# Performance work log

Measured on AMD Instinct MI355X. Metric: run time of the kernel, lower is better.

## Reference

```python
import jax, jax.numpy as jnp
import numpy as np

N_NODES = 100000
N_EDGES = 3200000
IN_FEAT = 256   # dim * decoder_heads = 128 * 2
HEADS = 2
N_CLASSES = 8
CURV = 1.0
NEG_SLOPE = 0.2
EPS = 1e-15


def setup_inputs() -> dict:
    key = jax.random.key(0)
    ks = jax.random.split(key, 7)
    x = jax.random.normal(ks[0], (N_NODES, IN_FEAT), dtype=jnp.float32) * 0.1
    edge_index = jax.random.randint(ks[1], (2, N_EDGES), 0, N_NODES, dtype=jnp.int64)
    W = jax.random.normal(ks[2], (IN_FEAT, HEADS * N_CLASSES), dtype=jnp.float32) * (1.0 / np.sqrt(IN_FEAT))
    attn_l = jax.random.normal(ks[3], (HEADS, N_CLASSES), dtype=jnp.float32) * 0.1
    attn_r = jax.random.normal(ks[4], (HEADS, N_CLASSES), dtype=jnp.float32) * 0.1
    bias = jnp.zeros((HEADS, N_CLASSES), dtype=jnp.float32)
    W_res = jax.random.normal(ks[5], (IN_FEAT, HEADS * N_CLASSES), dtype=jnp.float32) * (1.0 / np.sqrt(IN_FEAT))
    return {"x": x, "edge_index": edge_index, "W": W, "attn_l": attn_l,
            "attn_r": attn_r, "bias": bias, "W_res": W_res}


def _artanh(z):
    z = jnp.clip(z, -1.0 + 1e-7, 1.0 - 1e-7)
    return 0.5 * (jnp.log1p(z) - jnp.log1p(-z))


def _logmap0_poincare(x, c):
    # PoincareBall.logmap0; proj_tan0 is identity for the Poincare ball.
    sqrt_c = jnp.sqrt(c)
    norm = jnp.maximum(jnp.linalg.norm(x, axis=-1, keepdims=True), EPS)
    scale = _artanh(sqrt_c * norm) / (sqrt_c * norm)
    return scale * x


def reference(x, edge_index, W, attn_l, attn_r, bias, W_res):
    N = x.shape[0]
    # hyperbolic -> tangent space at origin
    h = _logmap0_poincare(x, CURV)                               # [N, F]
    # GATConv (DGL-style), dropout disabled (eval)
    feat = (h @ W).reshape(N, HEADS, N_CLASSES)                  # [N, H, C]
    el = jnp.einsum('nhc,hc->nh', feat, attn_l)                  # [N, H]
    er = jnp.einsum('nhc,hc->nh', feat, attn_r)                  # [N, H]
    src, dst = edge_index[0], edge_index[1]
    e = el[src] + er[dst]                                        # [E, H]
    e = jnp.where(e >= 0, e, NEG_SLOPE * e)                      # leaky_relu
    # edge softmax over incoming edges of each destination node
    m = jax.ops.segment_max(e, dst, num_segments=N)              # [N, H]
    m = jnp.where(jnp.isfinite(m), m, 0.0)
    e_exp = jnp.exp(e - m[dst])                                  # [E, H]
    denom = jax.ops.segment_sum(e_exp, dst, num_segments=N)      # [N, H]
    alpha = e_exp / jnp.maximum(denom[dst], EPS)                 # [E, H]
    # aggregate messages
    msg = alpha[:, :, None] * feat[src]                          # [E, H, C]
    rst = jax.ops.segment_sum(msg, dst, num_segments=N)          # [N, H, C]
    # residual + bias
    rst = rst + (h @ W_res).reshape(N, HEADS, N_CLASSES) + bias
    # Decoder.decode: probs.mean(dim=1) over heads
    return rst.mean(axis=1)                                      # [N, C]
```

## Files before the change

kernel.cpp:

```cpp
#include <hip/hip_runtime.h>
#include <math.h>

#define N_NODES 100000
#define N_EDGES 3200000
#define IN_FEAT 256
#define HEADS 2
#define NC 8
#define FH 16
#define NEG_SLOPE 0.2f
#define EPSF 1e-15f

#define BSH 7
#define BUCK_W 128
#define DLM 127
#define NBUCK ((N_NODES + BUCK_W - 1) / BUCK_W)
#define B1 256
#define EPB (N_EDGES / B1)

#define SORT_CAP 5120
#define RCAP (SORT_CAP / 256)

typedef float f32x4 __attribute__((ext_vector_type(4)));
typedef short bf16x8 __attribute__((ext_vector_type(8)));

__device__ __forceinline__ unsigned short f2bf(float f) {
    unsigned u = __float_as_uint(f);
    u += 0x7FFFu + ((u >> 16) & 1u);
    return (unsigned short)(u >> 16);
}
__device__ __forceinline__ float bflo(unsigned u) { return __uint_as_float(u << 16); }
__device__ __forceinline__ float bfhi(unsigned u) { return __uint_as_float(u & 0xFFFF0000u); }

__device__ __forceinline__ int chunk_of_block(int bid) {
    return (bid & 7) * (B1 / 8) + (bid >> 3);
}

__global__ __launch_bounds__(256) void k_node(
        const float* __restrict__ x, const float* __restrict__ W,
        const float* __restrict__ Wres, const float* __restrict__ attn_l,
        const float* __restrict__ attn_r,
        unsigned short* __restrict__ featb, float* __restrict__ res,
        float* __restrict__ el, float* __restrict__ er) {
    int wid = (blockIdx.x * 256 + threadIdx.x) >> 6;
    int n0 = wid * 16;
    if (n0 >= N_NODES) return;
    int l   = threadIdx.x & 63;
    int col = l & 15;
    int g   = l >> 4;

    bf16x8 bw[8], bq[8];
    #pragma unroll
    for (int kk = 0; kk < 8; kk++) {
        #pragma unroll
        for (int j = 0; j < 8; j++) {
            int k = kk * 32 + g * 8 + j;
            bw[kk][j] = (short)f2bf(W[k * FH + col]);
            bq[kk][j] = (short)f2bf(Wres[k * FH + col]);
        }
    }

    const float* xr = x + (size_t)(n0 + col) * IN_FEAT;
    f32x4 acc0 = {0.f, 0.f, 0.f, 0.f};
    f32x4 acc1 = {0.f, 0.f, 0.f, 0.f};
    float ss = 0.f;
    #pragma unroll
    for (int kk = 0; kk < 8; kk++) {
        float4 v0 = *(const float4*)(xr + kk * 32 + g * 8);
        float4 v1 = *(const float4*)(xr + kk * 32 + g * 8 + 4);
        ss += v0.x * v0.x + v0.y * v0.y + v0.z * v0.z + v0.w * v0.w
            + v1.x * v1.x + v1.y * v1.y + v1.z * v1.z + v1.w * v1.w;
        bf16x8 a;
        a[0] = (short)f2bf(v0.x); a[1] = (short)f2bf(v0.y);
        a[2] = (short)f2bf(v0.z); a[3] = (short)f2bf(v0.w);
        a[4] = (short)f2bf(v1.x); a[5] = (short)f2bf(v1.y);
        a[6] = (short)f2bf(v1.z); a[7] = (short)f2bf(v1.w);
        acc0 = __builtin_amdgcn_mfma_f32_16x16x32_bf16(a, bw[kk], acc0, 0, 0, 0);
        acc1 = __builtin_amdgcn_mfma_f32_16x16x32_bf16(a, bq[kk], acc1, 0, 0, 0);
    }

    ss += __shfl_xor(ss, 16);
    ss += __shfl_xor(ss, 32);
    float norm = fmaxf(sqrtf(ss), EPSF);
    float z = fminf(norm, 1.f - 1e-7f);
    float at = 0.5f * (log1pf(z) - log1pf(-z));
    float scale = at / norm;

    float alc = attn_l[col], arc = attn_r[col];

    #pragma unroll
    for (int i = 0; i < 4; i++) {
        int ri = g * 4 + i;
        float s_i = __shfl(scale, ri);
        int nr = n0 + ri;
        float f_i = acc0[i] * s_i;
        float q_i = acc1[i] * s_i;
        featb[(size_t)nr * FH + col] = f2bf(f_i);
        res  [(size_t)nr * FH + col] = q_i;
        float pl = f_i * alc, pr = f_i * arc;
        float pl0 = (col < 8) ? pl : 0.f, pl1 = (col < 8) ? 0.f : pl;
        float pr0 = (col < 8) ? pr : 0.f, pr1 = (col < 8) ? 0.f : pr;
        #pragma unroll
        for (int m = 1; m < 16; m <<= 1) {
            pl0 += __shfl_xor(pl0, m); pl1 += __shfl_xor(pl1, m);
            pr0 += __shfl_xor(pr0, m); pr1 += __shfl_xor(pr1, m);
        }
        if (col == 0) {
            *(float2*)(el + nr * 2) = make_float2(pl0, pl1);
            *(float2*)(er + nr * 2) = make_float2(pr0, pr1);
        }
    }
}

__global__ __launch_bounds__(256) void k_count(const int* __restrict__ ei,
                                               int* __restrict__ hist_g) {
    __shared__ int h[NBUCK];
    for (int i = threadIdx.x; i < NBUCK; i += 256) h[i] = 0;
    __syncthreads();
    int chunk = chunk_of_block(blockIdx.x);
    const int4* dp = (const int4*)(ei + N_EDGES + (size_t)chunk * EPB);
    for (int i = threadIdx.x; i < EPB / 4; i += 256) {
        int4 d = dp[i];
        atomicAdd(&h[d.x >> BSH], 1);
        atomicAdd(&h[d.y >> BSH], 1);
        atomicAdd(&h[d.z >> BSH], 1);
        atomicAdd(&h[d.w >> BSH], 1);
    }
    __syncthreads();
    int* outp = hist_g + (size_t)chunk * NBUCK;
    for (int i = threadIdx.x; i < NBUCK; i += 256) outp[i] = h[i];
}

__global__ __launch_bounds__(64) void k_scan1(int* __restrict__ hist_g,
                                              int* __restrict__ btot) {
    __shared__ int sm[64];
    int bucket = blockIdx.x;
    int t = threadIdx.x;
    int carry = 0;
    for (int base = 0; base < B1; base += 64) {
        int blk = base + t;
        int v = hist_g[(size_t)blk * NBUCK + bucket];
        __syncthreads();
        sm[t] = v;
        __syncthreads();
        for (int off = 1; off < 64; off <<= 1) {
            int u = (t >= off) ? sm[t - off] : 0;
            __syncthreads();
            sm[t] += u;
            __syncthreads();
        }
        hist_g[(size_t)blk * NBUCK + bucket] = carry + sm[t] - v;
        carry += sm[63];
    }
    if (t == 0) btot[bucket] = carry;
}

__global__ __launch_bounds__(1024) void k_scan2(const int* __restrict__ btot,
                                                int* __restrict__ bstart) {
    __shared__ int sm[1024];
    int t = threadIdx.x;
    int v = (t < NBUCK) ? btot[t] : 0;
    sm[t] = v;
    __syncthreads();
    for (int off = 1; off < 1024; off <<= 1) {
        int u = (t >= off) ? sm[t - off] : 0;
        __syncthreads();
        sm[t] += u;
        __syncthreads();
    }
    if (t < NBUCK) bstart[t] = sm[t] - v;
    if (t == 1023) bstart[NBUCK] = sm[1023];
}

__global__ __launch_bounds__(256) void k_scatter2(const int* __restrict__ ei,
                                                  const int* __restrict__ hist_g,
                                                  const int* __restrict__ bstart,
                                                  unsigned* __restrict__ packed) {
    __shared__ int cur[NBUCK];
    int chunk = chunk_of_block(blockIdx.x);
    const int* hrow = hist_g + (size_t)chunk * NBUCK;
    for (int i = threadIdx.x; i < NBUCK; i += 256) cur[i] = bstart[i] + hrow[i];
    __syncthreads();
    size_t e0 = (size_t)chunk * EPB;
    const int4* sp = (const int4*)(ei + e0);
    const int4* dp = (const int4*)(ei + N_EDGES + e0);
    for (int i = threadIdx.x; i < EPB / 4; i += 256) {
        int4 s = sp[i];
        int4 d = dp[i];
        int p0 = atomicAdd(&cur[d.x >> BSH], 1);
        int p1 = atomicAdd(&cur[d.y >> BSH], 1);
        int p2 = atomicAdd(&cur[d.z >> BSH], 1);
        int p3 = atomicAdd(&cur[d.w >> BSH], 1);
        packed[p0] = (unsigned)s.x | ((unsigned)(d.x & DLM) << 17);
        packed[p1] = (unsigned)s.y | ((unsigned)(d.y & DLM) << 17);
        packed[p2] = (unsigned)s.z | ((unsigned)(d.z & DLM) << 17);
        packed[p3] = (unsigned)s.w | ((unsigned)(d.w & DLM) << 17);
    }
}

__global__ __launch_bounds__(256) void k_aggsort(
        const unsigned* __restrict__ packed, const int* __restrict__ bstart,
        const float* __restrict__ el, const float* __restrict__ er,
        const unsigned short* __restrict__ featb, const float* __restrict__ res,
        const float* __restrict__ bias, float* __restrict__ out) {
    __shared__ int cnt[BUCK_W];
    __shared__ int off[BUCK_W];
    __shared__ unsigned srt[SORT_CAP];
    int b = blockIdx.x, t = threadIdx.x;
    int lo = bstart[b], hi = bstart[b + 1];

    if (t < BUCK_W) cnt[t] = 0;
    __syncthreads();

    unsigned pe[RCAP];
    int      tk[RCAP];
    #pragma unroll
    for (int i = 0; i < RCAP; i++) {
        int j = lo + i * 256 + t;
        if (j < hi) {
            unsigned p = packed[j];
            pe[i] = p;
            tk[i] = atomicAdd(&cnt[p >> 17], 1);
        } else {
            pe[i] = 0u; tk[i] = -1;
        }
    }
    __syncthreads();

    if (t < BUCK_W) off[t] = cnt[t];
    __syncthreads();
    #pragma unroll
    for (int d = 1; d < BUCK_W; d <<= 1) {
        int v = (t < BUCK_W && t >= d) ? off[t - d] : 0;
        __syncthreads();
        if (t < BUCK_W) off[t] += v;
        __syncthreads();
    }

    #pragma unroll
    for (int i = 0; i < RCAP; i++) {
        if (tk[i] >= 0) {
            int dl = (int)(pe[i] >> 17);
            srt[off[dl] - cnt[dl] + tk[i]] = pe[i] & 0x1FFFFu;
        }
    }
    __syncthreads();

    int dl = t >> 1, r = t & 1;
    int n = b * BUCK_W + dl;
    if (n >= N_NODES) return;
    int sBeg = off[dl] - cnt[dl];
    int sEnd = off[dl];
    float2 ern = *(const float2*)(er + n * 2);
    float den0 = 0.f, den1 = 0.f;
    float S[FH];
    #pragma unroll
    for (int k = 0; k < FH; k++) S[k] = 0.f;

    int j = sBeg + r;
    for (; j + 2 < sEnd; j += 4) {
        int sa = (int)srt[j], sb2 = (int)srt[j + 2];
        float2 ea = *(const float2*)(el + sa * 2);
        float2 eb = *(const float2*)(el + sb2 * 2);
        const uint4* fpa = (const uint4*)(featb + (size_t)sa * FH);
        const uint4* fpb = (const uint4*)(featb + (size_t)sb2 * FH);
        uint4 ua0 = fpa[0], ua1 = fpa[1];
        uint4 ub0 = fpb[0], ub1 = fpb[1];
        float va0 = ea.x + ern.x, va1 = ea.y + ern.y;
        float vb0 = eb.x + ern.x, vb1 = eb.y + ern.y;
        va0 = va0 >= 0.f ? va0 : NEG_SLOPE * va0;
        va1 = va1 >= 0.f ? va1 : NEG_SLOPE * va1;
        vb0 = vb0 >= 0.f ? vb0 : NEG_SLOPE * vb0;
        vb1 = vb1 >= 0.f ? vb1 : NEG_SLOPE * vb1;
        float wa0 = __expf(va0), wa1 = __expf(va1);
        float wb0 = __expf(vb0), wb1 = __expf(vb1);
        den0 += wa0 + wb0; den1 += wa1 + wb1;
        S[0]  = fmaf(wa0, bflo(ua0.x), fmaf(wb0, bflo(ub0.x), S[0]));
        S[1]  = fmaf(wa0, bfhi(ua0.x), fmaf(wb0, bfhi(ub0.x), S[1]));
        S[2]  = fmaf(wa0, bflo(ua0.y), fmaf(wb0, bflo(ub0.y), S[2]));
        S[3]  = fmaf(wa0, bfhi(ua0.y), fmaf(wb0, bfhi(ub0.y), S[3]));
        S[4]  = fmaf(wa0, bflo(ua0.z), fmaf(wb0, bflo(ub0.z), S[4]));
        S[5]  = fmaf(wa0, bfhi(ua0.z), fmaf(wb0, bfhi(ub0.z), S[5]));
        S[6]  = fmaf(wa0, bflo(ua0.w), fmaf(wb0, bflo(ub0.w), S[6]));
        S[7]  = fmaf(wa0, bfhi(ua0.w), fmaf(wb0, bfhi(ub0.w), S[7]));
        S[8]  = fmaf(wa1, bflo(ua1.x), fmaf(wb1, bflo(ub1.x), S[8]));
        S[9]  = fmaf(wa1, bfhi(ua1.x), fmaf(wb1, bfhi(ub1.x), S[9]));
        S[10] = fmaf(wa1, bflo(ua1.y), fmaf(wb1, bflo(ub1.y), S[10]));
        S[11] = fmaf(wa1, bfhi(ua1.y), fmaf(wb1, bfhi(ub1.y), S[11]));
        S[12] = fmaf(wa1, bflo(ua1.z), fmaf(wb1, bflo(ub1.z), S[12]));
        S[13] = fmaf(wa1, bfhi(ua1.z), fmaf(wb1, bfhi(ub1.z), S[13]));
        S[14] = fmaf(wa1, bflo(ua1.w), fmaf(wb1, bflo(ub1.w), S[14]));
        S[15] = fmaf(wa1, bfhi(ua1.w), fmaf(wb1, bfhi(ub1.w), S[15]));
    }
    for (; j < sEnd; j += 2) {
        int sa = (int)srt[j];
        float2 ea = *(const float2*)(el + sa * 2);
        float v0 = ea.x + ern.x, v1 = ea.y + ern.y;
        v0 = v0 >= 0.f ? v0 : NEG_SLOPE * v0;
        v1 = v1 >= 0.f ? v1 : NEG_SLOPE * v1;
        float w0 = __expf(v0), w1 = __expf(v1);
        den0 += w0; den1 += w1;
        const uint4* fp = (const uint4*)(featb + (size_t)sa * FH);
        uint4 u0 = fp[0], u1 = fp[1];
        S[0]  = fmaf(w0, bflo(u0.x), S[0]);  S[1]  = fmaf(w0, bfhi(u0.x), S[1]);
        S[2]  = fmaf(w0, bflo(u0.y), S[2]);  S[3]  = fmaf(w0, bfhi(u0.y), S[3]);
        S[4]  = fmaf(w0, bflo(u0.z), S[4]);  S[5]  = fmaf(w0, bfhi(u0.z), S[5]);
        S[6]  = fmaf(w0, bflo(u0.w), S[6]);  S[7]  = fmaf(w0, bfhi(u0.w), S[7]);
        S[8]  = fmaf(w1, bflo(u1.x), S[8]);  S[9]  = fmaf(w1, bfhi(u1.x), S[9]);
        S[10] = fmaf(w1, bflo(u1.y), S[10]); S[11] = fmaf(w1, bfhi(u1.y), S[11]);
        S[12] = fmaf(w1, bflo(u1.z), S[12]); S[13] = fmaf(w1, bfhi(u1.z), S[13]);
        S[14] = fmaf(w1, bflo(u1.w), S[14]); S[15] = fmaf(w1, bfhi(u1.w), S[15]);
    }

    #pragma unroll
    for (int k = 0; k < FH; k++) S[k] += __shfl_xor(S[k], 1);
    den0 += __shfl_xor(den0, 1);
    den1 += __shfl_xor(den1, 1);

    if (r == 0) {
        float inv0 = 1.f / fmaxf(den0, EPSF);
        float inv1 = 1.f / fmaxf(den1, EPSF);
        const float* rr = res + (size_t)n * FH;
        float4 r0a = *(const float4*)(rr + 0),  r0b = *(const float4*)(rr + 4);
        float4 r1a = *(const float4*)(rr + 8),  r1b = *(const float4*)(rr + 12);
        float4 oa, ob;
        oa.x = 0.5f * ((S[0] * inv0 + r0a.x + bias[0])  + (S[8]  * inv1 + r1a.x + bias[8]));
        oa.y = 0.5f * ((S[1] * inv0 + r0a.y + bias[1])  + (S[9]  * inv1 + r1a.y + bias[9]));
        oa.z = 0.5f * ((S[2] * inv0 + r0a.z + bias[2])  + (S[10] * inv1 + r1a.z + bias[10]));
        oa.w = 0.5f * ((S[3] * inv0 + r0a.w + bias[3])  + (S[11] * inv1 + r1a.w + bias[11]));
        ob.x = 0.5f * ((S[4] * inv0 + r0b.x + bias[4])  + (S[12] * inv1 + r1b.x + bias[12]));
        ob.y = 0.5f * ((S[5] * inv0 + r0b.y + bias[5])  + (S[13] * inv1 + r1b.y + bias[13]));
        ob.z = 0.5f * ((S[6] * inv0 + r0b.z + bias[6])  + (S[14] * inv1 + r1b.z + bias[14]));
        ob.w = 0.5f * ((S[7] * inv0 + r0b.w + bias[7])  + (S[15] * inv1 + r1b.w + bias[15]));
        *(float4*)(out + (size_t)n * NC + 0) = oa;
        *(float4*)(out + (size_t)n * NC + 4) = ob;
    }
}

extern "C" void kernel_launch(void* const* d_in, const int* in_sizes, int n_in,
                              void* d_out, int out_size, void* d_ws, size_t ws_size,
                              hipStream_t stream) {
    const float* x      = (const float*)d_in[0];
    const int*   ei     = (const int*)d_in[1];
    const float* W      = (const float*)d_in[2];
    const float* attn_l = (const float*)d_in[3];
    const float* attn_r = (const float*)d_in[4];
    const float* bias   = (const float*)d_in[5];
    const float* Wres   = (const float*)d_in[6];
    float* out = (float*)d_out;

    char* ws = (char*)d_ws;
    const size_t szFB   = (size_t)N_NODES * FH * sizeof(unsigned short);
    const size_t szNF   = (size_t)N_NODES * FH * sizeof(float);
    const size_t szNH   = (size_t)N_NODES * HEADS * sizeof(float);
    const size_t szHist = (((size_t)B1 * NBUCK * sizeof(int)) + 255) & ~(size_t)255;
    const size_t szBt   = 4096;
    size_t off = 0;
    unsigned short* featb = (unsigned short*)(ws + off); off += szFB;
    float*    res    = (float*)(ws + off); off += szNF;
    float*    el     = (float*)(ws + off); off += szNH;
    float*    er     = (float*)(ws + off); off += szNH;
    int*      hist_g = (int*)  (ws + off); off += szHist;
    int*      btot   = (int*)  (ws + off); off += szBt;
    int*      bstart = (int*)  (ws + off); off += szBt;
    unsigned* packed = (unsigned*)(ws + off); off += (size_t)N_EDGES * sizeof(unsigned);

    k_node<<<(N_NODES / 16 + 3) / 4, 256, 0, stream>>>(x, W, Wres, attn_l, attn_r,
                                                       featb, res, el, er);
    k_count<<<B1, 256, 0, stream>>>(ei, hist_g);
    k_scan1<<<NBUCK, 64, 0, stream>>>(hist_g, btot);
    k_scan2<<<1, 1024, 0, stream>>>(btot, bstart);
    k_scatter2<<<B1, 256, 0, stream>>>(ei, hist_g, bstart, packed);
    k_aggsort<<<NBUCK, 256, 0, stream>>>(packed, bstart, el, er, featb, res, bias, out);
}
```

Before: 117.2 us.

## Halve destination bucket width and use four threads per destination node

Destination buckets shrink from 128 to 64 nodes, which doubles the bucket count and the number of aggregation blocks. Inside the aggregation kernel each node now gets four threads instead of two, with a two-step shuffle reduction. The bucket scan is widened to 2048 entries and the histogram and scatter scale with the new count. The intent is more parallelism and latency hiding in the gather-heavy aggregation, at the cost of a larger histogram, more scatter atomics, extra shuffles, and a smaller per-bucket sort capacity that could overflow.

```diff
diff --git a/kernel.cpp b/kernel.cpp
--- a/kernel.cpp
+++ b/kernel.cpp
@@ -10,15 +10,16 @@
 #define NEG_SLOPE 0.2f
 #define EPSF 1e-15f
 
-#define BSH 7
-#define BUCK_W 128
-#define DLM 127
+#define BSH 6
+#define BUCK_W 64
+#define DLM 63
 #define NBUCK ((N_NODES + BUCK_W - 1) / BUCK_W)
 #define B1 256
 #define EPB (N_EDGES / B1)
 
-#define SORT_CAP 5120
+#define SORT_CAP 2560
 #define RCAP (SORT_CAP / 256)
+#define TPD 4
 
 typedef float f32x4 __attribute__((ext_vector_type(4)));
 typedef short bf16x8 __attribute__((ext_vector_type(8)));
@@ -156,19 +157,23 @@
 
 __global__ __launch_bounds__(1024) void k_scan2(const int* __restrict__ btot,
                                                 int* __restrict__ bstart) {
-    __shared__ int sm[1024];
+    __shared__ int sm[2048];
     int t = threadIdx.x;
-    int v = (t < NBUCK) ? btot[t] : 0;
-    sm[t] = v;
-    __syncthreads();
-    for (int off = 1; off < 1024; off <<= 1) {
-        int u = (t >= off) ? sm[t - off] : 0;
-        __syncthreads();
-        sm[t] += u;
-        __syncthreads();
-    }
-    if (t < NBUCK) bstart[t] = sm[t] - v;
-    if (t == 1023) bstart[NBUCK] = sm[1023];
+    int i0 = t, i1 = t + 1024;
+    int v0 = (i0 < NBUCK) ? btot[i0] : 0;
+    int v1 = (i1 < NBUCK) ? btot[i1] : 0;
+    sm[i0] = v0; sm[i1] = v1;
+    __syncthreads();
+    for (int d = 1; d < 2048; d <<= 1) {
+        int a0 = (i0 >= d) ? sm[i0 - d] : 0;
+        int a1 = (i1 >= d) ? sm[i1 - d] : 0;
+        __syncthreads();
+        sm[i0] += a0; sm[i1] += a1;
+        __syncthreads();
+    }
+    if (i0 < NBUCK) bstart[i0] = sm[i0] - v0;
+    if (i1 < NBUCK) bstart[i1] = sm[i1] - v1;
+    if (t == 0) bstart[NBUCK] = sm[2047];
 }
 
 __global__ __launch_bounds__(256) void k_scatter2(const int* __restrict__ ei,
@@ -245,7 +250,7 @@
     }
     __syncthreads();
 
-    int dl = t >> 1, r = t & 1;
+    int dl = t >> 2, r = t & 3;
     int n = b * BUCK_W + dl;
     if (n >= N_NODES) return;
     int sBeg = off[dl] - cnt[dl];
@@ -257,8 +262,8 @@
     for (int k = 0; k < FH; k++) S[k] = 0.f;
 
     int j = sBeg + r;
-    for (; j + 2 < sEnd; j += 4) {
-        int sa = (int)srt[j], sb2 = (int)srt[j + 2];
+    for (; j + TPD < sEnd; j += 2 * TPD) {
+        int sa = (int)srt[j], sb2 = (int)srt[j + TPD];
         float2 ea = *(const float2*)(el + sa * 2);
         float2 eb = *(const float2*)(el + sb2 * 2);
         const uint4* fpa = (const uint4*)(featb + (size_t)sa * FH);
@@ -291,7 +296,7 @@
         S[14] = fmaf(wa1, bflo(ua1.w), fmaf(wb1, bflo(ub1.w), S[14]));
         S[15] = fmaf(wa1, bfhi(ua1.w), fmaf(wb1, bfhi(ub1.w), S[15]));
     }
-    for (; j < sEnd; j += 2) {
+    for (; j < sEnd; j += TPD) {
         int sa = (int)srt[j];
         float2 ea = *(const float2*)(el + sa * 2);
         float v0 = ea.x + ern.x, v1 = ea.y + ern.y;
@@ -312,9 +317,12 @@
     }
 
     #pragma unroll
-    for (int k = 0; k < FH; k++) S[k] += __shfl_xor(S[k], 1);
-    den0 += __shfl_xor(den0, 1);
-    den1 += __shfl_xor(den1, 1);
+    for (int k = 0; k < FH; k++) {
+        S[k] += __shfl_xor(S[k], 1);
+        S[k] += __shfl_xor(S[k], 2);
+    }
+    den0 += __shfl_xor(den0, 1); den0 += __shfl_xor(den0, 2);
+    den1 += __shfl_xor(den1, 1); den1 += __shfl_xor(den1, 2);
 
     if (r == 0) {
         float inv0 = 1.f / fmaxf(den0, EPSF);
@@ -353,7 +361,7 @@
     const size_t szNF   = (size_t)N_NODES * FH * sizeof(float);
     const size_t szNH   = (size_t)N_NODES * HEADS * sizeof(float);
     const size_t szHist = (((size_t)B1 * NBUCK * sizeof(int)) + 255) & ~(size_t)255;
-    const size_t szBt   = 4096;
+    const size_t szBt   = 8192;
     size_t off = 0;
     unsigned short* featb = (unsigned short*)(ws + off); off += szFB;
     float*    res    = (float*)(ws + off); off += szNF;
```

Measured after the change: 112.3 us. -4.2%, faster.
